# Kernel optimization log

Measured on AMD Instinct MI355X. Metric: run time of the kernel, lower is better.

The kernel has to match this reference:

```python
import jax, jax.numpy as jnp
import numpy as np

N_NODES = 50000
N_EDGES = 800000
D_NODE = 64
D_EDGE = 32
UNITS = 64
HEADS1 = 4
OUT_DIM = 1


def setup_inputs() -> dict:
    key = jax.random.key(0)
    ks = jax.random.split(key, 20)
    s = lambda fan_in: 1.0 / np.sqrt(fan_in)
    inp = {
        'node_feats': jax.random.normal(ks[0], (N_NODES, D_NODE), jnp.float32),
        'edge_feats': jax.random.normal(ks[1], (N_EDGES, D_EDGE), jnp.float32),
        'senders': jax.random.randint(ks[2], (N_EDGES,), 0, N_NODES, jnp.int32),
        'receivers': jax.random.randint(ks[3], (N_EDGES,), 0, N_NODES, jnp.int32),
        # layer 1 (heads=4, per_head=16)
        'Wq1': jax.random.normal(ks[4], (D_NODE, UNITS), jnp.float32) * s(D_NODE),
        'Ws1': jax.random.normal(ks[5], (D_NODE, UNITS), jnp.float32) * s(D_NODE),
        'We1': jax.random.normal(ks[6], (D_EDGE, UNITS), jnp.float32) * s(D_EDGE),
        'a1': jax.random.normal(ks[7], (HEADS1, UNITS // HEADS1), jnp.float32) * s(UNITS // HEADS1),
        'Wn1': jax.random.normal(ks[8], (D_NODE + UNITS, UNITS), jnp.float32) * s(D_NODE + UNITS),
        'bn1': jnp.zeros((UNITS,), jnp.float32),
        # layer 2 (heads=1, per_head=units)
        'Wq2': jax.random.normal(ks[9], (UNITS, UNITS), jnp.float32) * s(UNITS),
        'Ws2': jax.random.normal(ks[10], (UNITS, UNITS), jnp.float32) * s(UNITS),
        'We2': jax.random.normal(ks[11], (D_EDGE, UNITS), jnp.float32) * s(D_EDGE),
        'a2': jax.random.normal(ks[12], (1, UNITS), jnp.float32) * s(UNITS),
        'Wn2': jax.random.normal(ks[13], (UNITS + UNITS, UNITS), jnp.float32) * s(UNITS + UNITS),
        'bn2': jnp.zeros((UNITS,), jnp.float32),
        # readout
        'Wd': jax.random.normal(ks[14], (UNITS, OUT_DIM), jnp.float32) * s(UNITS),
        'bd': jnp.zeros((OUT_DIM,), jnp.float32),
    }
    return inp


def _gatv2_conv(h, e, senders, receivers, Wq, Ws, We, a, heads, ch):
    """TF-GNN GATv2Conv with sender_edge_feature: key = Ws h_j + We e_ij,
    logit = a . leaky_relu(Wq h_i + key), segment softmax over receiver,
    message = key * alpha, segment-sum to receiver, relu, merge heads."""
    n_nodes = h.shape[0]
    n_edges = senders.shape[0]
    q = (h @ Wq)[receivers].reshape(n_edges, heads, ch)      # gather receiver
    k = ((h @ Ws)[senders] + e @ We).reshape(n_edges, heads, ch)
    feat = jax.nn.leaky_relu(q + k, negative_slope=0.2)
    logits = jnp.einsum('ehc,hc->eh', feat, a)               # [E, H]
    m = jax.ops.segment_max(logits, receivers, num_segments=n_nodes)
    ex = jnp.exp(logits - m[receivers])
    denom = jax.ops.segment_sum(ex, receivers, num_segments=n_nodes)
    alpha = ex / denom[receivers]                            # segment softmax
    msg = (k * alpha[..., None]).reshape(n_edges, heads * ch)
    pooled = jax.ops.segment_sum(msg, receivers, num_segments=n_nodes)
    return jax.nn.relu(pooled)                               # [N, H*C]


def reference(node_feats, edge_feats, senders, receivers,
              Wq1, Ws1, We1, a1, Wn1, bn1,
              Wq2, Ws2, We2, a2, Wn2, bn2, Wd, bd):
    h = node_feats
    conv1 = _gatv2_conv(h, edge_feats, senders, receivers, Wq1, Ws1, We1, a1,
                        HEADS1, UNITS // HEADS1)
    h = jax.nn.relu(jnp.concatenate([h, conv1], axis=-1) @ Wn1 + bn1)
    conv2 = _gatv2_conv(h, edge_feats, senders, receivers, Wq2, Ws2, We2, a2,
                        1, UNITS)
    h = jax.nn.relu(jnp.concatenate([h, conv2], axis=-1) @ Wn2 + bn2)
    return h @ Wd + bd
```

## Files before the change

### kernel.cpp

```cpp
#include <hip/hip_runtime.h>
#include <hip/hip_bf16.h>

#define NNODES 50000
#define NEDGES 800000
#define UNITS 64
#define NTILES (NNODES/16)
#define NB_SCAN ((NNODES+255)/256)
#define NB_GEMM (NEDGES/16/4)
#define NB_NODE ((NTILES+3)/4)
#define NB_HIST ((NEDGES+255)/256)

typedef unsigned short ushort;
typedef unsigned int uint;
typedef __attribute__((ext_vector_type(8))) short bf16x8;
typedef __attribute__((ext_vector_type(4))) float floatx4;
typedef __attribute__((ext_vector_type(4))) ushort ushort4_t;

__device__ __forceinline__ ushort f2bf(float x){
  union{float f; uint u;} v; v.f = x;
  uint r = v.u + 0x7fffu + ((v.u >> 16) & 1u);
  return (ushort)(r >> 16);
}
__device__ __forceinline__ float bf2f(ushort h){
  union{uint u; float f;} v; v.u = ((uint)h) << 16; return v.f;
}
__device__ __forceinline__ void split8(const float* __restrict__ p, bf16x8& hi, bf16x8& lo){
  #pragma unroll
  for (int j=0;j<8;++j){
    float x = p[j];
    ushort h = f2bf(x);
    hi[j] = (short)h;
    lo[j] = (short)f2bf(x - bf2f(h));
  }
}

template<int CTRL>
__device__ __forceinline__ float dpp_add(float x){
  int y = __builtin_amdgcn_update_dpp(0, __float_as_int(x), CTRL, 0xF, 0xF, true);
  return x + __int_as_float(y);
}
template<int CH>
__device__ __forceinline__ float lane_sum(float p){
  p = dpp_add<0xB1>(p);
  p = dpp_add<0x4E>(p);
  p = dpp_add<0x141>(p);
  p = dpp_add<0x140>(p);
  if (CH == 64){
    p += __shfl_xor(p, 16);
    p += __shfl_xor(p, 32);
  }
  return p;
}


__device__ __forceinline__ void packunit(const float* __restrict__ W, int r8, int col,
                                         ushort* __restrict__ H, ushort* __restrict__ L){
  bf16x8 hi, lo;
  #pragma unroll
  for (int j=0;j<8;++j){
    float x = W[(r8*8+j)*64 + col];
    ushort h = f2bf(x);
    hi[j] = (short)h;
    lo[j] = (short)f2bf(x - bf2f(h));
  }
  *(bf16x8*)(H + ((size_t)r8*64 + col)*8) = hi;
  *(bf16x8*)(L + ((size_t)r8*64 + col)*8) = lo;
}


__global__ void k_init(const int* __restrict__ recv, int* __restrict__ counts,
                       const float* __restrict__ Wq1, const float* __restrict__ Ws1,
                       const float* __restrict__ Wn1, const float* __restrict__ Wq2,
                       const float* __restrict__ Ws2, const float* __restrict__ Wn2,
                       const float* __restrict__ We1, const float* __restrict__ We2,
                       ushort* __restrict__ wsp){
  if (blockIdx.x < NB_HIST){
    int e = blockIdx.x*blockDim.x + threadIdx.x;
    if (e < NEDGES) atomicAdd(&counts[recv[e]], 1);
    return;
  }
  int u = (blockIdx.x - NB_HIST)*blockDim.x + threadIdx.x;
  if (u >= 4608) return;
  ushort* p = wsp;
  const float* W; int base;
  if      (u < 512){  W=Wq1; base=u;        p += 0;      packunit(W, base>>6, base&63, p, p+4096); return; }
  else if (u < 1024){ W=Ws1; base=u-512;    p += 8192;   packunit(W, base>>6, base&63, p, p+4096); return; }
  else if (u < 2048){ W=Wn1; base=u-1024;   p += 16384;  packunit(W, base>>6, base&63, p, p+8192); return; }
  else if (u < 2560){ W=Wq2; base=u-2048;   p += 32768;  packunit(W, base>>6, base&63, p, p+4096); return; }
  else if (u < 3072){ W=Ws2; base=u-2560;   p += 40960;  packunit(W, base>>6, base&63, p, p+4096); return; }
  else if (u < 4096){ W=Wn2; base=u-3072;   p += 49152;  packunit(W, base>>6, base&63, p, p+8192); return; }
  else if (u < 4352){ W=We1; base=u-4096;   p += 65536;  packunit(W, base>>6, base&63, p, p+2048); return; }
  else {              W=We2; base=u-4352;   p += 69632;  packunit(W, base>>6, base&63, p, p+2048); return; }
}


__global__ void k_blocksum(const int* __restrict__ counts, int* __restrict__ bsum){
  __shared__ int red[256];
  int b = blockIdx.x, t = threadIdx.x;
  int i = b*256 + t;
  red[t] = (i < NNODES) ? counts[i] : 0;
  __syncthreads();
  for (int s=128; s>0; s>>=1){ if (t<s) red[t]+=red[t+s]; __syncthreads(); }
  if (t==0) bsum[b] = red[0];
}

__global__ void k_scantop(const int* __restrict__ bsum, int* __restrict__ bscan,
                          int* __restrict__ offsets){
  __shared__ int sh[256];
  int t = threadIdx.x;
  int own = (t < NB_SCAN) ? bsum[t] : 0;
  sh[t] = own;
  __syncthreads();
  for (int s=1; s<256; s<<=1){
    int u = (t>=s) ? sh[t-s] : 0;
    __syncthreads();
    sh[t] += u;
    __syncthreads();
  }
  if (t < NB_SCAN) bscan[t] = sh[t] - own;
  if (t == 0) offsets[NNODES] = sh[NB_SCAN-1];
}

__global__ void k_scanfinal(const int* __restrict__ counts, const int* __restrict__ bscan,
                            int* __restrict__ offsets, int* __restrict__ cursor){
  __shared__ int sh[256];
  int b = blockIdx.x, t = threadIdx.x;
  int i = b*256 + t;
  int own = (i < NNODES) ? counts[i] : 0;
  sh[t] = own;
  __syncthreads();
  for (int s=1; s<256; s<<=1){
    int u = (t>=s) ? sh[t-s] : 0;
    __syncthreads();
    sh[t] += u;
    __syncthreads();
  }
  if (i < NNODES){
    int excl = bscan[b] + sh[t] - own;
    offsets[i] = excl; cursor[i] = excl;
  }
}

__global__ void k_scatter(const int* __restrict__ recv, const int* __restrict__ send,
                          int* __restrict__ cursor, int* __restrict__ sorted_eid,
                          int* __restrict__ ssend){
  int e = blockIdx.x*blockDim.x + threadIdx.x;
  if (e < NEDGES){
    int pos = atomicAdd(&cursor[recv[e]], 1);
    sorted_eid[pos] = e;
    ssend[pos] = send[e];
  }
}

__global__ void k_permute(const float* __restrict__ ef, const int* __restrict__ sorted_eid,
                          ushort* __restrict__ efh){
  int t = blockIdx.x*blockDim.x + threadIdx.x;
  if (t >= NEDGES*8) return;
  int i = t >> 3, d4 = t & 7;
  int e = sorted_eid[i];
  float4 x = *(const float4*)(ef + (size_t)e*32 + d4*4);
  ushort4_t o;
  o.x = f2bf(x.x); o.y = f2bf(x.y); o.z = f2bf(x.z); o.w = f2bf(x.w);
  *(ushort4_t*)(efh + (size_t)i*32 + d4*4) = o;
}


__global__ void k_mme(const ushort* __restrict__ efh,
                      const ushort* __restrict__ WeH, const ushort* __restrict__ WeL,
                      ushort* __restrict__ E,
                      const float* __restrict__ h,
                      const ushort* __restrict__ WqH, const ushort* __restrict__ WqL,
                      const ushort* __restrict__ WsH, const ushort* __restrict__ WsL,
                      float* __restrict__ Q, ushort* __restrict__ Sb){
  int tid = threadIdx.x;
  int lane = tid & 63;
  int m = lane & 15, quad = lane >> 4;

  if (blockIdx.x < NB_GEMM){
    int tile = blockIdx.x*4 + (tid >> 6);
    size_t base = (size_t)tile * 16;
    const bf16x8 ah = *(const bf16x8*)(efh + (base + m)*32 + quad*8);
    #pragma unroll
    for (int t4 = 0; t4 < 4; ++t4){
      size_t fo = ((size_t)quad*64 + t4*16 + m)*8;
      const bf16x8 bh = *(const bf16x8*)(WeH + fo);
      const bf16x8 bl = *(const bf16x8*)(WeL + fo);
      floatx4 acc = {0.f,0.f,0.f,0.f};
      acc = __builtin_amdgcn_mfma_f32_16x16x32_bf16(ah, bl, acc, 0, 0, 0);
      acc = __builtin_amdgcn_mfma_f32_16x16x32_bf16(ah, bh, acc, 0, 0, 0);
      #pragma unroll
      for (int r = 0; r < 4; ++r)
        E[(base + quad*4 + r)*64 + t4*16 + m] = f2bf(acc[r]);
    }
    return;
  }

  int tile = (int)(blockIdx.x - NB_GEMM)*4 + (tid>>6);
  if (tile >= NTILES) return;
  size_t base = (size_t)tile*16;
  floatx4 accQ[4], accS[4];
  #pragma unroll
  for (int t=0;t<4;++t){ accQ[t]=(floatx4){0,0,0,0}; accS[t]=(floatx4){0,0,0,0}; }
  #pragma unroll
  for (int ks=0; ks<2; ++ks){
    bf16x8 ah, al;
    split8(h + (base+m)*64 + ks*32 + quad*8, ah, al);
    int r8 = ks*4 + quad;
    #pragma unroll
    for (int t4=0;t4<4;++t4){
      size_t fo = ((size_t)r8*64 + t4*16 + m)*8;
      const bf16x8 bh = *(const bf16x8*)(WqH + fo);
      const bf16x8 bl = *(const bf16x8*)(WqL + fo);
      const bf16x8 ch = *(const bf16x8*)(WsH + fo);
      const bf16x8 cl = *(const bf16x8*)(WsL + fo);
      accQ[t4] = __builtin_amdgcn_mfma_f32_16x16x32_bf16(al, bh, accQ[t4],0,0,0);
      accQ[t4] = __builtin_amdgcn_mfma_f32_16x16x32_bf16(ah, bl, accQ[t4],0,0,0);
      accQ[t4] = __builtin_amdgcn_mfma_f32_16x16x32_bf16(ah, bh, accQ[t4],0,0,0);
      accS[t4] = __builtin_amdgcn_mfma_f32_16x16x32_bf16(al, ch, accS[t4],0,0,0);
      accS[t4] = __builtin_amdgcn_mfma_f32_16x16x32_bf16(ah, cl, accS[t4],0,0,0);
      accS[t4] = __builtin_amdgcn_mfma_f32_16x16x32_bf16(ah, ch, accS[t4],0,0,0);
    }
  }
  #pragma unroll
  for (int t4=0;t4<4;++t4)
    #pragma unroll
    for (int r=0;r<4;++r){
      size_t row = base + quad*4 + r;
      Q[row*64 + t4*16 + m]  = accQ[t4][r];
      Sb[row*64 + t4*16 + m] = f2bf(accS[t4][r]);
    }
}


template<int H>
__global__ void k_pool(const int* __restrict__ offsets, const int* __restrict__ ssend,
                       const float* __restrict__ Q, const ushort* __restrict__ Sb,
                       const ushort* __restrict__ E, const float* __restrict__ a,
                       float* __restrict__ conv){
  int tid = threadIdx.x;
  int n = blockIdx.x*4 + (tid>>6);
  uint c = tid & 63;
  if (n >= NNODES) return;
  constexpr int CH = 64 / H;
  float av = a[c] * 1.4426950408889634f;
  float q = Q[(uint)n*64 + c];
  int beg = offsets[n], end = offsets[n+1];
  float lsum[8], asum[8];
  #pragma unroll
  for (int u=0;u<8;++u){ lsum[u]=0.f; asum[u]=0.f; }
  int i = beg;
  for (; i + 7 < end; i += 8){
    float k[8];
    #pragma unroll
    for (int u=0;u<8;++u){
      uint s = (uint)ssend[i+u];
      k[u] = bf2f(Sb[s*64u + c]) + bf2f(E[(uint)(i+u)*64u + c]);
    }
    #pragma unroll
    for (int u=0;u<8;++u){
      float f = q + k[u];
      f = fmaxf(f, 0.2f*f);
      float w = exp2f(lane_sum<CH>(f*av));
      lsum[u] += w;
      asum[u] = fmaf(w, k[u], asum[u]);
    }
  }
  if (i + 3 < end){
    float k[4];
    #pragma unroll
    for (int u=0;u<4;++u){
      uint s = (uint)ssend[i+u];
      k[u] = bf2f(Sb[s*64u + c]) + bf2f(E[(uint)(i+u)*64u + c]);
    }
    #pragma unroll
    for (int u=0;u<4;++u){
      float f = q + k[u];
      f = fmaxf(f, 0.2f*f);
      float w = exp2f(lane_sum<CH>(f*av));
      lsum[u] += w;
      asum[u] = fmaf(w, k[u], asum[u]);
    }
    i += 4;
  }
  for (; i < end; ++i){
    uint s = (uint)ssend[i];
    float k0 = bf2f(Sb[s*64u + c]) + bf2f(E[(uint)i*64u + c]);
    float f = q + k0;
    f = fmaxf(f, 0.2f*f);
    float w = exp2f(lane_sum<CH>(f*av));
    lsum[0] += w;
    asum[0] = fmaf(w, k0, asum[0]);
  }
  float l   = ((lsum[0]+lsum[1])+(lsum[2]+lsum[3])) + ((lsum[4]+lsum[5])+(lsum[6]+lsum[7]));
  float acc = ((asum[0]+asum[1])+(asum[2]+asum[3])) + ((asum[4]+asum[5])+(asum[6]+asum[7]));
  float res = (l > 0.f) ? acc/l : 0.f;
  conv[(uint)n*64 + c] = fmaxf(res, 0.f);
}


template<bool READOUT>
__global__ void k_update(const float* __restrict__ h, const float* __restrict__ conv,
                         const ushort* __restrict__ WnH, const ushort* __restrict__ WnL,
                         const float* __restrict__ bn,
                         float* __restrict__ hout, const float* __restrict__ Wd,
                         const float* __restrict__ bd, float* __restrict__ out){
  int tid = threadIdx.x;
  int tile = blockIdx.x*4 + (tid>>6);
  if (tile >= NTILES) return;
  int lane = tid & 63;
  int m = lane & 15, quad = lane >> 4;
  size_t base = (size_t)tile*16;
  floatx4 acc[4];
  #pragma unroll
  for (int t=0;t<4;++t) acc[t]=(floatx4){0,0,0,0};
  #pragma unroll
  for (int ks=0; ks<4; ++ks){
    bf16x8 ah, al;
    const float* src = (ks < 2) ? (h    + (base+m)*64 + ks*32     + quad*8)
                                : (conv + (base+m)*64 + (ks-2)*32 + quad*8);
    split8(src, ah, al);
    int r8 = ks*4 + quad;
    #pragma unroll
    for (int t4=0;t4<4;++t4){
      size_t fo = ((size_t)r8*64 + t4*16 + m)*8;
      const bf16x8 bh = *(const bf16x8*)(WnH + fo);
      const bf16x8 bl = *(const bf16x8*)(WnL + fo);
      acc[t4] = __builtin_amdgcn_mfma_f32_16x16x32_bf16(al, bh, acc[t4],0,0,0);
      acc[t4] = __builtin_amdgcn_mfma_f32_16x16x32_bf16(ah, bl, acc[t4],0,0,0);
      acc[t4] = __builtin_amdgcn_mfma_f32_16x16x32_bf16(ah, bh, acc[t4],0,0,0);
    }
  }
  if (!READOUT){
    #pragma unroll
    for (int t4=0;t4<4;++t4){
      float b = bn[t4*16 + m];
      #pragma unroll
      for (int r=0;r<4;++r)
        hout[(base + quad*4 + r)*64 + t4*16 + m] = fmaxf(acc[t4][r] + b, 0.f);
    }
  } else {
    float bv[4], wd[4];
    #pragma unroll
    for (int t4=0;t4<4;++t4){ bv[t4] = bn[t4*16+m]; wd[t4] = Wd[t4*16+m]; }
    #pragma unroll
    for (int r=0;r<4;++r){
      float v = 0.f;
      #pragma unroll
      for (int t4=0;t4<4;++t4) v += fmaxf(acc[t4][r] + bv[t4], 0.f) * wd[t4];
      #pragma unroll
      for (int off=1; off<16; off<<=1) v += __shfl_xor(v, off);
      if (m == 0) out[base + quad*4 + r] = v + bd[0];
    }
  }
}

extern "C" void kernel_launch(void* const* d_in, const int* in_sizes, int n_in,
                              void* d_out, int out_size, void* d_ws, size_t ws_size,
                              hipStream_t stream){
  const float* node_feats = (const float*)d_in[0];
  const float* edge_feats = (const float*)d_in[1];
  const int*   senders    = (const int*)d_in[2];
  const int*   receivers  = (const int*)d_in[3];
  const float* Wq1 = (const float*)d_in[4];
  const float* Ws1 = (const float*)d_in[5];
  const float* We1 = (const float*)d_in[6];
  const float* a1  = (const float*)d_in[7];
  const float* Wn1 = (const float*)d_in[8];
  const float* bn1 = (const float*)d_in[9];
  const float* Wq2 = (const float*)d_in[10];
  const float* Ws2 = (const float*)d_in[11];
  const float* We2 = (const float*)d_in[12];
  const float* a2  = (const float*)d_in[13];
  const float* Wn2 = (const float*)d_in[14];
  const float* bn2 = (const float*)d_in[15];
  const float* Wd  = (const float*)d_in[16];
  const float* bd  = (const float*)d_in[17];
  float* out = (float*)d_out;

  char* base = (char*)d_ws;
  const size_t NF = (size_t)NNODES*64;
  float*  Q    = (float*)base;  base += NF*4;
  ushort* Sb   = (ushort*)base; base += NF*2;
  float*  conv = (float*)base;  base += NF*4;
  float*  h1   = (float*)base;  base += NF*4;
  ushort* efh  = (ushort*)base; base += (size_t)NEDGES*32*2;
  ushort* E    = (ushort*)base; base += (size_t)NEDGES*64*2;
  int* counts     = (int*)base; base += (size_t)NNODES*4;
  int* offsets    = (int*)base; base += (size_t)(NNODES+1)*4;
  int* cursor     = (int*)base; base += (size_t)NNODES*4;
  int* sorted_eid = (int*)base; base += (size_t)NEDGES*4;
  int* ssend      = (int*)base; base += (size_t)NEDGES*4;
  ushort* wsp     = (ushort*)base; base += (size_t)73728*2;
  int* bsum       = (int*)base; base += (size_t)NB_SCAN*4;
  int* bscan      = (int*)base; base += (size_t)NB_SCAN*4;

  if (ws_size < (size_t)(base - (char*)d_ws)) return;

  const ushort *Wq1H=wsp+0,     *Wq1L=wsp+4096,  *Ws1H=wsp+8192,  *Ws1L=wsp+12288;
  const ushort *Wn1H=wsp+16384, *Wn1L=wsp+24576, *Wq2H=wsp+32768, *Wq2L=wsp+36864;
  const ushort *Ws2H=wsp+40960, *Ws2L=wsp+45056, *Wn2H=wsp+49152, *Wn2L=wsp+57344;
  const ushort *We1H=wsp+65536, *We1L=wsp+67584, *We2H=wsp+69632, *We2L=wsp+71680;

  dim3 b256(256);
  int nb_node = (NNODES+3)/4;
  int nb_edge = (NEDGES+255)/256;

  hipMemsetAsync(counts, 0, (size_t)NNODES*4, stream);
  k_init     <<<NB_HIST + (4608+255)/256, b256, 0, stream>>>(receivers, counts,
                Wq1,Ws1,Wn1,Wq2,Ws2,Wn2,We1,We2, wsp);
  k_blocksum <<<NB_SCAN, b256, 0, stream>>>(counts, bsum);
  k_scantop  <<<1, b256, 0, stream>>>(bsum, bscan, offsets);
  k_scanfinal<<<NB_SCAN, b256, 0, stream>>>(counts, bscan, offsets, cursor);
  k_scatter  <<<nb_edge, b256, 0, stream>>>(receivers, senders, cursor, sorted_eid, ssend);
  k_permute  <<<(NEDGES*8+255)/256, b256, 0, stream>>>(edge_feats, sorted_eid, efh);

  k_mme <<<NB_GEMM+NB_NODE, b256, 0, stream>>>(efh, We1H, We1L, E,
          node_feats, Wq1H,Wq1L, Ws1H,Ws1L, Q, Sb);
  k_pool<4> <<<nb_node, b256, 0, stream>>>(offsets, ssend, Q, Sb, E, a1, conv);
  k_update<false><<<NB_NODE, b256, 0, stream>>>(node_feats, conv, Wn1H, Wn1L, bn1, h1,
                                                nullptr, nullptr, nullptr);

  k_mme <<<NB_GEMM+NB_NODE, b256, 0, stream>>>(efh, We2H, We2L, E,
          h1, Wq2H,Wq2L, Ws2H,Ws2L, Q, Sb);
  k_pool<1> <<<nb_node, b256, 0, stream>>>(offsets, ssend, Q, Sb, E, a2, conv);
  k_update<true><<<NB_NODE, b256, 0, stream>>>(h1, conv, Wn2H, Wn2L, bn2, nullptr,
                                               Wd, bd, out);
}
```

Baseline: 485.1 us.

## Fuse edge-feature projection into pooling kernel, drop permute and E buffers

Removes the separate permute kernel and the per-edge E = e@We GEMM that wrote a 64-wide bf16 tensor per edge. The pooling kernel now gathers raw fp32 edge features by sorted edge id, converts them to bf16, and computes the projection with MFMA per 16-edge chunk into LDS, then reads it from there. This avoids writing and re-reading about 100MB of E per layer and the efh staging buffer. In exchange the edge features are gathered randomly in each layer and the MFMA work is done even for partial chunks of nodes with small degree, which wastes lanes for nodes with ~16 incoming edges. There is no syncthreads around the LDS round-trip, but each wave only touches its own LDS slice.

```diff
diff --git a/kernel.cpp b/kernel.cpp
--- a/kernel.cpp
+++ b/kernel.cpp
@@ -6,7 +6,6 @@
 #define UNITS 64
 #define NTILES (NNODES/16)
 #define NB_SCAN ((NNODES+255)/256)
-#define NB_GEMM (NEDGES/16/4)
 #define NB_NODE ((NTILES+3)/4)
 #define NB_HIST ((NEDGES+255)/256)
 
@@ -152,50 +151,15 @@
   }
 }
 
-__global__ void k_permute(const float* __restrict__ ef, const int* __restrict__ sorted_eid,
-                          ushort* __restrict__ efh){
-  int t = blockIdx.x*blockDim.x + threadIdx.x;
-  if (t >= NEDGES*8) return;
-  int i = t >> 3, d4 = t & 7;
-  int e = sorted_eid[i];
-  float4 x = *(const float4*)(ef + (size_t)e*32 + d4*4);
-  ushort4_t o;
-  o.x = f2bf(x.x); o.y = f2bf(x.y); o.z = f2bf(x.z); o.w = f2bf(x.w);
-  *(ushort4_t*)(efh + (size_t)i*32 + d4*4) = o;
-}
-
-
-__global__ void k_mme(const ushort* __restrict__ efh,
-                      const ushort* __restrict__ WeH, const ushort* __restrict__ WeL,
-                      ushort* __restrict__ E,
-                      const float* __restrict__ h,
-                      const ushort* __restrict__ WqH, const ushort* __restrict__ WqL,
-                      const ushort* __restrict__ WsH, const ushort* __restrict__ WsL,
-                      float* __restrict__ Q, ushort* __restrict__ Sb){
+
+__global__ void k_qs(const float* __restrict__ h,
+                     const ushort* __restrict__ WqH, const ushort* __restrict__ WqL,
+                     const ushort* __restrict__ WsH, const ushort* __restrict__ WsL,
+                     float* __restrict__ Q, ushort* __restrict__ Sb){
   int tid = threadIdx.x;
   int lane = tid & 63;
   int m = lane & 15, quad = lane >> 4;
-
-  if (blockIdx.x < NB_GEMM){
-    int tile = blockIdx.x*4 + (tid >> 6);
-    size_t base = (size_t)tile * 16;
-    const bf16x8 ah = *(const bf16x8*)(efh + (base + m)*32 + quad*8);
-    #pragma unroll
-    for (int t4 = 0; t4 < 4; ++t4){
-      size_t fo = ((size_t)quad*64 + t4*16 + m)*8;
-      const bf16x8 bh = *(const bf16x8*)(WeH + fo);
-      const bf16x8 bl = *(const bf16x8*)(WeL + fo);
-      floatx4 acc = {0.f,0.f,0.f,0.f};
-      acc = __builtin_amdgcn_mfma_f32_16x16x32_bf16(ah, bl, acc, 0, 0, 0);
-      acc = __builtin_amdgcn_mfma_f32_16x16x32_bf16(ah, bh, acc, 0, 0, 0);
-      #pragma unroll
-      for (int r = 0; r < 4; ++r)
-        E[(base + quad*4 + r)*64 + t4*16 + m] = f2bf(acc[r]);
-    }
-    return;
-  }
-
-  int tile = (int)(blockIdx.x - NB_GEMM)*4 + (tid>>6);
+  int tile = blockIdx.x*4 + (tid>>6);
   if (tile >= NTILES) return;
   size_t base = (size_t)tile*16;
   floatx4 accQ[4], accS[4];
@@ -234,62 +198,103 @@
 
 template<int H>
 __global__ void k_pool(const int* __restrict__ offsets, const int* __restrict__ ssend,
+                       const int* __restrict__ seid,
                        const float* __restrict__ Q, const ushort* __restrict__ Sb,
-                       const ushort* __restrict__ E, const float* __restrict__ a,
-                       float* __restrict__ conv){
+                       const float* __restrict__ ef,
+                       const ushort* __restrict__ WeH, const ushort* __restrict__ WeL,
+                       const float* __restrict__ a, float* __restrict__ conv){
+  __shared__ float Elds[4][16*66];
   int tid = threadIdx.x;
   int n = blockIdx.x*4 + (tid>>6);
   uint c = tid & 63;
   if (n >= NNODES) return;
+  float* El = Elds[tid>>6];
+  int m = (int)(c & 15), quad = (int)(c >> 4);
   constexpr int CH = 64 / H;
   float av = a[c] * 1.4426950408889634f;
   float q = Q[(uint)n*64 + c];
+
+  bf16x8 BH[4], BL[4];
+  #pragma unroll
+  for (int t4=0;t4<4;++t4){
+    size_t fo = ((size_t)quad*64 + t4*16 + m)*8;
+    BH[t4] = *(const bf16x8*)(WeH + fo);
+    BL[t4] = *(const bf16x8*)(WeL + fo);
+  }
+
   int beg = offsets[n], end = offsets[n+1];
   float lsum[8], asum[8];
   #pragma unroll
   for (int u=0;u<8;++u){ lsum[u]=0.f; asum[u]=0.f; }
-  int i = beg;
-  for (; i + 7 < end; i += 8){
-    float k[8];
-    #pragma unroll
-    for (int u=0;u<8;++u){
+
+  for (int i = beg; i < end; i += 16){
+    int cnt = end - i; if (cnt > 16) cnt = 16;
+
+    bf16x8 ah = (bf16x8){0,0,0,0,0,0,0,0};
+    if (m < cnt){
+      uint e = (uint)seid[i+m];
+      const float* src = ef + (size_t)e*32 + quad*8;
+      float4 x0 = *(const float4*)(src);
+      float4 x1 = *(const float4*)(src+4);
+      ah[0]=(short)f2bf(x0.x); ah[1]=(short)f2bf(x0.y);
+      ah[2]=(short)f2bf(x0.z); ah[3]=(short)f2bf(x0.w);
+      ah[4]=(short)f2bf(x1.x); ah[5]=(short)f2bf(x1.y);
+      ah[6]=(short)f2bf(x1.z); ah[7]=(short)f2bf(x1.w);
+    }
+
+    #pragma unroll
+    for (int t4=0;t4<4;++t4){
+      floatx4 acc = {0.f,0.f,0.f,0.f};
+      acc = __builtin_amdgcn_mfma_f32_16x16x32_bf16(ah, BL[t4], acc, 0,0,0);
+      acc = __builtin_amdgcn_mfma_f32_16x16x32_bf16(ah, BH[t4], acc, 0,0,0);
+      #pragma unroll
+      for (int r=0;r<4;++r)
+        El[(quad*4+r)*66 + t4*16 + m] = acc[r];
+    }
+
+    int u = 0;
+    for (; u+7 < cnt; u += 8){
+      float k8[8];
+      #pragma unroll
+      for (int t=0;t<8;++t){
+        uint s = (uint)ssend[i+u+t];
+        k8[t] = bf2f(Sb[s*64u + c]) + El[(u+t)*66 + c];
+      }
+      #pragma unroll
+      for (int t=0;t<8;++t){
+        float f = q + k8[t];
+        f = fmaxf(f, 0.2f*f);
+        float w = exp2f(lane_sum<CH>(f*av));
+        lsum[t] += w;
+        asum[t] = fmaf(w, k8[t], asum[t]);
+      }
+    }
+    if (u+3 < cnt){
+      float k4[4];
+      #pragma unroll
+      for (int t=0;t<4;++t){
+        uint s = (uint)ssend[i+u+t];
+        k4[t] = bf2f(Sb[s*64u + c]) + El[(u+t)*66 + c];
+      }
+      #pragma unroll
+      for (int t=0;t<4;++t){
+        float f = q + k4[t];
+        f = fmaxf(f, 0.2f*f);
+        float w = exp2f(lane_sum<CH>(f*av));
+        lsum[t] += w;
+        asum[t] = fmaf(w, k4[t], asum[t]);
+      }
+      u += 4;
+    }
+    for (; u < cnt; ++u){
       uint s = (uint)ssend[i+u];
-      k[u] = bf2f(Sb[s*64u + c]) + bf2f(E[(uint)(i+u)*64u + c]);
-    }
-    #pragma unroll
-    for (int u=0;u<8;++u){
-      float f = q + k[u];
+      float k0 = bf2f(Sb[s*64u + c]) + El[u*66 + c];
+      float f = q + k0;
       f = fmaxf(f, 0.2f*f);
       float w = exp2f(lane_sum<CH>(f*av));
-      lsum[u] += w;
-      asum[u] = fmaf(w, k[u], asum[u]);
-    }
-  }
-  if (i + 3 < end){
-    float k[4];
-    #pragma unroll
-    for (int u=0;u<4;++u){
-      uint s = (uint)ssend[i+u];
-      k[u] = bf2f(Sb[s*64u + c]) + bf2f(E[(uint)(i+u)*64u + c]);
-    }
-    #pragma unroll
-    for (int u=0;u<4;++u){
-      float f = q + k[u];
-      f = fmaxf(f, 0.2f*f);
-      float w = exp2f(lane_sum<CH>(f*av));
-      lsum[u] += w;
-      asum[u] = fmaf(w, k[u], asum[u]);
-    }
-    i += 4;
-  }
-  for (; i < end; ++i){
-    uint s = (uint)ssend[i];
-    float k0 = bf2f(Sb[s*64u + c]) + bf2f(E[(uint)i*64u + c]);
-    float f = q + k0;
-    f = fmaxf(f, 0.2f*f);
-    float w = exp2f(lane_sum<CH>(f*av));
-    lsum[0] += w;
-    asum[0] = fmaf(w, k0, asum[0]);
+      lsum[0] += w;
+      asum[0] = fmaf(w, k0, asum[0]);
+    }
   }
   float l   = ((lsum[0]+lsum[1])+(lsum[2]+lsum[3])) + ((lsum[4]+lsum[5])+(lsum[6]+lsum[7]));
   float acc = ((asum[0]+asum[1])+(asum[2]+asum[3])) + ((asum[4]+asum[5])+(asum[6]+asum[7]));
@@ -383,8 +388,6 @@
   ushort* Sb   = (ushort*)base; base += NF*2;
   float*  conv = (float*)base;  base += NF*4;
   float*  h1   = (float*)base;  base += NF*4;
-  ushort* efh  = (ushort*)base; base += (size_t)NEDGES*32*2;
-  ushort* E    = (ushort*)base; base += (size_t)NEDGES*64*2;
   int* counts     = (int*)base; base += (size_t)NNODES*4;
   int* offsets    = (int*)base; base += (size_t)(NNODES+1)*4;
   int* cursor     = (int*)base; base += (size_t)NNODES*4;
@@ -412,17 +415,16 @@
   k_scantop  <<<1, b256, 0, stream>>>(bsum, bscan, offsets);
   k_scanfinal<<<NB_SCAN, b256, 0, stream>>>(counts, bscan, offsets, cursor);
   k_scatter  <<<nb_edge, b256, 0, stream>>>(receivers, senders, cursor, sorted_eid, ssend);
-  k_permute  <<<(NEDGES*8+255)/256, b256, 0, stream>>>(edge_feats, sorted_eid, efh);
-
-  k_mme <<<NB_GEMM+NB_NODE, b256, 0, stream>>>(efh, We1H, We1L, E,
-          node_feats, Wq1H,Wq1L, Ws1H,Ws1L, Q, Sb);
-  k_pool<4> <<<nb_node, b256, 0, stream>>>(offsets, ssend, Q, Sb, E, a1, conv);
+
+  k_qs <<<NB_NODE, b256, 0, stream>>>(node_feats, Wq1H,Wq1L, Ws1H,Ws1L, Q, Sb);
+  k_pool<4> <<<nb_node, b256, 0, stream>>>(offsets, ssend, sorted_eid, Q, Sb,
+                                           edge_feats, We1H, We1L, a1, conv);
   k_update<false><<<NB_NODE, b256, 0, stream>>>(node_feats, conv, Wn1H, Wn1L, bn1, h1,
                                                 nullptr, nullptr, nullptr);
 
-  k_mme <<<NB_GEMM+NB_NODE, b256, 0, stream>>>(efh, We2H, We2L, E,
-          h1, Wq2H,Wq2L, Ws2H,Ws2L, Q, Sb);
-  k_pool<1> <<<nb_node, b256, 0, stream>>>(offsets, ssend, Q, Sb, E, a2, conv);
+  k_qs <<<NB_NODE, b256, 0, stream>>>(h1, Wq2H,Wq2L, Ws2H,Ws2L, Q, Sb);
+  k_pool<1> <<<nb_node, b256, 0, stream>>>(offsets, ssend, sorted_eid, Q, Sb,
+                                           edge_feats, We2H, We2L, a2, conv);
   k_update<true><<<NB_NODE, b256, 0, stream>>>(h1, conv, Wn2H, Wn2L, bn2, nullptr,
                                                Wd, bd, out);
 }
```

Measured after the change: 499.3 us. 1.03x slower.
